# Performance work log

Measured on AMD Instinct MI355X. Metric: run time of the kernel, lower is better.

The kernel has to match this reference:

```python
import jax, jax.numpy as jnp
import numpy as np

EMBEDDING_DIM = 64
NUM_EMBEDDINGS = 1024
BETA = 0.25


def setup_inputs() -> dict:
    key = jax.random.key(0)
    k1, k2 = jax.random.split(key)
    inputs = jax.random.normal(k1, (64, 32, 32, EMBEDDING_DIM), dtype=jnp.float32)
    rand_range = 1.0 / NUM_EMBEDDINGS
    embeddings = jax.random.uniform(
        k2, (EMBEDDING_DIM, NUM_EMBEDDINGS),
        minval=-rand_range, maxval=rand_range, dtype=jnp.float32)
    return {"inputs": inputs, "embeddings": embeddings}


def reference(inputs, embeddings):
    # Flatten to [N, D]
    flat = inputs.reshape(-1, EMBEDDING_DIM)
    distances = (jnp.sum(flat ** 2, axis=1, keepdims=True)
                 - 2.0 * (flat @ embeddings)
                 + jnp.sum(embeddings ** 2, axis=0, keepdims=True))  # [N, K]
    encoding_indices = jnp.argmax(-distances, axis=1)
    encoding_indices = encoding_indices.reshape(inputs.shape[:-1])
    # Embedding lookup: codebook is [D, K], gather columns
    quantized = embeddings.T[encoding_indices]  # [..., D]
    e_latent_loss = jnp.mean((jax.lax.stop_gradient(quantized) - inputs) ** 2)
    q_latent_loss = jnp.mean((quantized - jax.lax.stop_gradient(inputs)) ** 2)
    loss = e_latent_loss + q_latent_loss * BETA
    # Straight-through estimator
    quantized = inputs + jax.lax.stop_gradient(quantized - inputs)
    return (quantized, loss, encoding_indices)
```

## Files before the change

kernel.cpp:

```cpp
#include <hip/hip_runtime.h>
#include <math.h>

#define EMB_D 64
#define EMB_K 1024
#define NROWS 65536
#define QELEMS (NROWS * EMB_D)


__global__ __launch_bounds__(256) void prep_kernel(const float* __restrict__ E,
                                                   float* __restrict__ Et,
                                                   float* __restrict__ esq,
                                                   double* lsum) {
    int k = blockIdx.x * 256 + threadIdx.x;
    if (k == 0) *lsum = 0.0;
    if (k >= EMB_K) return;
    float s = 0.f;
#pragma unroll
    for (int d = 0; d < EMB_D; ++d) {
        float v = E[d * EMB_K + k];
        Et[k * EMB_D + d] = v;
        s = fmaf(v, v, s);
    }
    esq[k] = s;
}

#define DOT4(acc, q, e)                                    \
    do {                                                   \
        acc = fmaf((q).x, (e).x, acc);                     \
        acc = fmaf((q).y, (e).y, acc);                     \
        acc = fmaf((q).z, (e).z, acc);                     \
        acc = fmaf((q).w, (e).w, acc);                     \
    } while (0)

#define PIN4(v) asm volatile("" : "+v"((v).x), "+v"((v).y), "+v"((v).z), "+v"((v).w))

__global__ __launch_bounds__(256, 2) void main_kernel(const float* X,
                                                      const float* __restrict__ Et,
                                                      const float* __restrict__ esq,
                                                      float* __restrict__ quant,
                                                      float* __restrict__ idxf,
                                                      double* lsum) {
    __shared__ float sd[4][64];
    __shared__ int   si[4][64];
    __shared__ int   sidx[64];

    const int lane = threadIdx.x & 63;
    const int w    = threadIdx.x >> 6;
    const int rowbase = blockIdx.x * 64;

    const float4* xr = reinterpret_cast<const float4*>(X + (size_t)(rowbase + lane) * EMB_D);
    float4 x0 = xr[0],  x1 = xr[1],  x2 = xr[2],  x3 = xr[3];
    float4 x4 = xr[4],  x5 = xr[5],  x6 = xr[6],  x7 = xr[7];
    float4 x8 = xr[8],  x9 = xr[9],  x10 = xr[10], x11 = xr[11];
    float4 x12 = xr[12], x13 = xr[13], x14 = xr[14], x15 = xr[15];

    float xsq = 0.f;
    DOT4(xsq, x0, x0);   DOT4(xsq, x1, x1);   DOT4(xsq, x2, x2);   DOT4(xsq, x3, x3);
    DOT4(xsq, x4, x4);   DOT4(xsq, x5, x5);   DOT4(xsq, x6, x6);   DOT4(xsq, x7, x7);
    DOT4(xsq, x8, x8);   DOT4(xsq, x9, x9);   DOT4(xsq, x10, x10); DOT4(xsq, x11, x11);
    DOT4(xsq, x12, x12); DOT4(xsq, x13, x13); DOT4(xsq, x14, x14); DOT4(xsq, x15, x15);

    PIN4(x0);  PIN4(x1);  PIN4(x2);  PIN4(x3);
    PIN4(x4);  PIN4(x5);  PIN4(x6);  PIN4(x7);
    PIN4(x8);  PIN4(x9);  PIN4(x10); PIN4(x11);
    PIN4(x12); PIN4(x13); PIN4(x14); PIN4(x15);

    const int k0 = __builtin_amdgcn_readfirstlane(w) * (EMB_K / 4);

    float bestd = INFINITY;
    int   besti = 0;
    for (int k = k0; k < k0 + EMB_K / 4; k += 2) {
        const float4* e0 = reinterpret_cast<const float4*>(Et + (size_t)k * EMB_D);
        const float4* e1 = e0 + 16;
        float d0 = 0.f, d1 = 0.f;
#define STEP(i) { float4 a = e0[i]; float4 b = e1[i]; DOT4(d0, x##i, a); DOT4(d1, x##i, b); }
        STEP(0)  STEP(1)  STEP(2)  STEP(3)
        STEP(4)  STEP(5)  STEP(6)  STEP(7)
        STEP(8)  STEP(9)  STEP(10) STEP(11)
        STEP(12) STEP(13) STEP(14) STEP(15)
#undef STEP
        float dist0 = (xsq - 2.0f * d0) + esq[k];
        float dist1 = (xsq - 2.0f * d1) + esq[k + 1];
        if (dist0 < bestd) { bestd = dist0; besti = k; }
        if (dist1 < bestd) { bestd = dist1; besti = k + 1; }
    }
    sd[w][lane] = bestd;
    si[w][lane] = besti;
    __syncthreads();

    if (threadIdx.x < 64) {
        float bd = sd[0][lane];
        int   bi = si[0][lane];
#pragma unroll
        for (int u = 1; u < 4; ++u) {
            if (sd[u][lane] < bd) { bd = sd[u][lane]; bi = si[u][lane]; }
        }
        sidx[lane] = bi;
        idxf[rowbase + lane] = (float)bi;
    }
    __syncthreads();

    {
        const int r = threadIdx.x >> 2;
        const int p = threadIdx.x & 3;
        const int k = sidx[r];
        const float4* xq = reinterpret_cast<const float4*>(X + (size_t)(rowbase + r) * EMB_D) + p * 4;
        const float4* qq = reinterpret_cast<const float4*>(Et + (size_t)k * EMB_D) + p * 4;
        float4*       oq = reinterpret_cast<float4*>(quant + (size_t)(rowbase + r) * EMB_D) + p * 4;
        float ps = 0.f;
#pragma unroll
        for (int u = 0; u < 4; ++u) {
            float4 xx = xq[u];
            float4 q  = qq[u];
            float dx = q.x - xx.x, dy = q.y - xx.y, dz = q.z - xx.z, dw = q.w - xx.w;
            oq[u] = make_float4(xx.x + dx, xx.y + dy, xx.z + dz, xx.w + dw);
            ps += dx * dx + dy * dy + dz * dz + dw * dw;
        }
#pragma unroll
        for (int off = 32; off > 0; off >>= 1) ps += __shfl_down(ps, off, 64);
        if (lane == 0) atomicAdd(lsum, (double)ps);
    }
}

__global__ void finalize_kernel(const double* lsum, float* loss_out) {
    double m = *lsum / (double)QELEMS;
    *loss_out = (float)(m + 0.25 * m);
}

extern "C" void kernel_launch(void* const* d_in, const int* in_sizes, int n_in,
                              void* d_out, int out_size, void* d_ws, size_t ws_size,
                              hipStream_t stream) {
    const float* X = (const float*)d_in[0];
    const float* E = (const float*)d_in[1];

    float* out = (float*)d_out;
    float* quant = out;
    float* loss  = out + QELEMS;
    float* idxf  = out + QELEMS + 1;

    char* ws = (char*)d_ws;
    float*  Et   = (float*)(ws);
    float*  esq  = (float*)(ws + 262144);
    double* lsum = (double*)(ws + 266240);

    prep_kernel<<<4, 256, 0, stream>>>(E, Et, esq, lsum);
    main_kernel<<<NROWS / 64, 256, 0, stream>>>(X, Et, esq, quant, idxf, lsum);
    finalize_kernel<<<1, 1, 0, stream>>>(lsum, loss);
}
```

Before: 241.5 us.

## Feed codebook via scalar registers with inline-asm FMAs and tile the transpose

The distance loop now reads each codebook row as wave-uniform scalar operands and feeds them directly into v_fmac_f32 inline assembly. This replaces per-lane vector global loads of the same data, which should cut vector memory traffic and VGPR pressure. The prep kernel now transposes through an LDS tile so its global reads and writes are coalesced. Risks: the scalar loads depend on the compiler producing SGPRs for the asm 's' constraints, and the loop now handles one code per iteration with a single serial accumulator chain, which reduces ILP.

New measurement: 240.9 us. Within noise of the previous version (-0.2%).

```diff
diff --git a/kernel.cpp b/kernel.cpp
--- a/kernel.cpp
+++ b/kernel.cpp
@@ -11,17 +11,27 @@
                                                    float* __restrict__ Et,
                                                    float* __restrict__ esq,
                                                    double* lsum) {
-    int k = blockIdx.x * 256 + threadIdx.x;
-    if (k == 0) *lsum = 0.0;
-    if (k >= EMB_K) return;
-    float s = 0.f;
+    __shared__ float tile[256][65];
+    const int t = threadIdx.x;
+    const int kbase = blockIdx.x * 256;
+    if (blockIdx.x == 0 && t == 0) *lsum = 0.0;
+
 #pragma unroll
-    for (int d = 0; d < EMB_D; ++d) {
-        float v = E[d * EMB_K + k];
-        Et[k * EMB_D + d] = v;
-        s = fmaf(v, v, s);
+    for (int d = 0; d < EMB_D; ++d) tile[t][d] = E[d * EMB_K + kbase + t];
+    __syncthreads();
+
+    {
+        float s = 0.f;
+#pragma unroll
+        for (int d = 0; d < EMB_D; ++d) { float v = tile[t][d]; s = fmaf(v, v, s); }
+        esq[kbase + t] = s;
     }
-    esq[k] = s;
+
+#pragma unroll
+    for (int j = 0; j < EMB_D; ++j) {
+        int m = j * 256 + t;
+        Et[(size_t)kbase * EMB_D + m] = tile[m >> 6][m & 63];
+    }
 }
 
 #define DOT4(acc, q, e)                                    \
@@ -33,6 +43,22 @@
     } while (0)
 
 #define PIN4(v) asm volatile("" : "+v"((v).x), "+v"((v).y), "+v"((v).z), "+v"((v).w))
+
+#define FMA8(acc, E, B, va, vb)                                              \
+    asm("v_fmac_f32 %0, %1, %9\n\t"                                          \
+        "v_fmac_f32 %0, %2, %10\n\t"                                         \
+        "v_fmac_f32 %0, %3, %11\n\t"                                         \
+        "v_fmac_f32 %0, %4, %12\n\t"                                         \
+        "v_fmac_f32 %0, %5, %13\n\t"                                         \
+        "v_fmac_f32 %0, %6, %14\n\t"                                         \
+        "v_fmac_f32 %0, %7, %15\n\t"                                         \
+        "v_fmac_f32 %0, %8, %16"                                             \
+        : "+v"(acc)                                                          \
+        : "s"((E)[(B) + 0]), "s"((E)[(B) + 1]), "s"((E)[(B) + 2]),           \
+          "s"((E)[(B) + 3]), "s"((E)[(B) + 4]), "s"((E)[(B) + 5]),           \
+          "s"((E)[(B) + 6]), "s"((E)[(B) + 7]),                              \
+          "v"((va).x), "v"((va).y), "v"((va).z), "v"((va).w),                \
+          "v"((vb).x), "v"((vb).y), "v"((vb).z), "v"((vb).w))
 
 __global__ __launch_bounds__(256, 2) void main_kernel(const float* X,
                                                       const float* __restrict__ Et,
@@ -64,25 +90,25 @@
     PIN4(x4);  PIN4(x5);  PIN4(x6);  PIN4(x7);
     PIN4(x8);  PIN4(x9);  PIN4(x10); PIN4(x11);
     PIN4(x12); PIN4(x13); PIN4(x14); PIN4(x15);
+    __syncthreads();
 
     const int k0 = __builtin_amdgcn_readfirstlane(w) * (EMB_K / 4);
 
     float bestd = INFINITY;
     int   besti = 0;
-    for (int k = k0; k < k0 + EMB_K / 4; k += 2) {
-        const float4* e0 = reinterpret_cast<const float4*>(Et + (size_t)k * EMB_D);
-        const float4* e1 = e0 + 16;
-        float d0 = 0.f, d1 = 0.f;
-#define STEP(i) { float4 a = e0[i]; float4 b = e1[i]; DOT4(d0, x##i, a); DOT4(d1, x##i, b); }
-        STEP(0)  STEP(1)  STEP(2)  STEP(3)
-        STEP(4)  STEP(5)  STEP(6)  STEP(7)
-        STEP(8)  STEP(9)  STEP(10) STEP(11)
-        STEP(12) STEP(13) STEP(14) STEP(15)
-#undef STEP
-        float dist0 = (xsq - 2.0f * d0) + esq[k];
-        float dist1 = (xsq - 2.0f * d1) + esq[k + 1];
-        if (dist0 < bestd) { bestd = dist0; besti = k; }
-        if (dist1 < bestd) { bestd = dist1; besti = k + 1; }
+    for (int k = k0; k < k0 + EMB_K / 4; ++k) {
+        const float* e = Et + (size_t)k * EMB_D;
+        float acc = 0.f;
+        FMA8(acc, e, 0,  x0,  x1);
+        FMA8(acc, e, 8,  x2,  x3);
+        FMA8(acc, e, 16, x4,  x5);
+        FMA8(acc, e, 24, x6,  x7);
+        FMA8(acc, e, 32, x8,  x9);
+        FMA8(acc, e, 40, x10, x11);
+        FMA8(acc, e, 48, x12, x13);
+        FMA8(acc, e, 56, x14, x15);
+        float dist = (xsq - 2.0f * acc) + esq[k];
+        if (dist < bestd) { bestd = dist; besti = k; }
     }
     sd[w][lane] = bestd;
     si[w][lane] = besti;
@@ -143,7 +169,7 @@
     float*  esq  = (float*)(ws + 262144);
     double* lsum = (double*)(ws + 266240);
 
-    prep_kernel<<<4, 256, 0, stream>>>(E, Et, esq, lsum);
+    prep_kernel<<<EMB_K / 256, 256, 0, stream>>>(E, Et, esq, lsum);
     main_kernel<<<NROWS / 64, 256, 0, stream>>>(X, Et, esq, quant, idxf, lsum);
     finalize_kernel<<<1, 1, 0, stream>>>(lsum, loss);
 }
```
